# Optimization experiments

Measured on AMD Instinct MI355X. Metric: run time of the kernel, lower is better.

## Reference

```python
import jax, jax.numpy as jnp
import numpy as np

NUM_CAPSULE = 10
DIM_CAPSULE = 16
ROUTINGS = 3
EPS = 1e-7  # K.epsilon()


def squash(x, axis=-1):
    # bojone squash: x / sqrt(s2 + eps) * s2 / (1 + s2)
    s2 = jnp.sum(jnp.square(x), axis=axis, keepdims=True)
    return x * s2 / ((1.0 + s2) * jnp.sqrt(s2 + EPS))


def setup_inputs() -> dict:
    key = jax.random.key(0)
    k1, k2 = jax.random.split(key)
    B, N, D_in = 64, 2048, 128  # batch, input_num_capsule, input_dim_capsule
    u_vecs = jax.random.normal(k1, (B, N, D_in), dtype=jnp.float32)
    fan_out = NUM_CAPSULE * DIM_CAPSULE
    limit = float(np.sqrt(6.0 / (D_in + fan_out)))  # glorot_uniform
    W = jax.random.uniform(k2, (D_in, fan_out), dtype=jnp.float32,
                           minval=-limit, maxval=limit)
    return {"u_vecs": u_vecs, "W": W}


def reference(u_vecs, W):
    B, N, _ = u_vecs.shape
    # share_weights=True: conv1d with kernel size 1 == matmul over feature dim
    u_hat = (u_vecs @ W).reshape(B, N, NUM_CAPSULE, DIM_CAPSULE)
    u_hat = jnp.transpose(u_hat, (0, 2, 1, 3))  # (B, J, N, D)
    b = jnp.zeros((B, NUM_CAPSULE, N), dtype=u_vecs.dtype)
    o = jnp.zeros((B, NUM_CAPSULE, DIM_CAPSULE), dtype=u_vecs.dtype)
    for i in range(ROUTINGS):
        c = jax.nn.softmax(b, axis=1)           # softmax over output capsules
        o = jnp.einsum('bjn,bjnd->bjd', c, u_hat)
        if i < ROUTINGS - 1:
            b = jnp.einsum('bjd,bjnd->bjn', o, u_hat)  # agreement update
    return squash(o)
```

## Files before the change

### kernel.cpp

```cpp
#include <hip/hip_runtime.h>
#include <math.h>


#define BATCH 64
#define NN    2048
#define KD    128
#define JCAP  10
#define DCAP  16
#define JDIM  160
#define EPSQ  1e-7f
#define TPB   256

#define WS_SP   0
#define WS_GP1  65536
#define WS_O2P  720896
#define WS_V0   802816
#define WS_V1   884736
#define WS_CNT  966656

__global__ __launch_bounds__(TPB) void k_prep(const float* __restrict__ u,
                                              float* __restrict__ Sp,
                                              unsigned int* __restrict__ cnt) {
  const int b = blockIdx.y, tile = blockIdx.x, t = threadIdx.x;
  if (b == 0 && tile == 0 && t < BATCH) cnt[t] = 0u;
  const int k4 = (t & 31) * 4, rg = t >> 5;
  __shared__ float4 red[256];
  const float* p = u + ((size_t)(b * NN) + tile * 256 + rg * 32) * KD + k4;
  float4 a = make_float4(0.f, 0.f, 0.f, 0.f);
#pragma unroll 4
  for (int r = 0; r < 32; ++r) {
    float4 w = *(const float4*)(p + (size_t)r * KD);
    a.x += w.x; a.y += w.y; a.z += w.z; a.w += w.w;
  }
  red[t] = a;
  __syncthreads();
  if (t < 32) {
    float4 s4 = red[t];
#pragma unroll
    for (int rg2 = 1; rg2 < 8; ++rg2) {
      float4 w = red[rg2 * 32 + t];
      s4.x += w.x; s4.y += w.y; s4.z += w.z; s4.w += w.w;
    }
    *(float4*)&Sp[(size_t)(b * 8 + tile) * KD + t * 4] = s4;
  }
}

__global__ __launch_bounds__(TPB) void k_makeV(const float* __restrict__ ws,
                                               const float* __restrict__ W,
                                               float* __restrict__ V,
                                               int pass) {
  const int b = blockIdx.x, t = threadIdx.x;
  __shared__ float gsum[JCAP * KD];
  __shared__ float o_s[JDIM];
  if (pass == 0) {
    const float* SpB = ws + WS_SP + (size_t)b * 8 * KD;
    if (t < KD) {
      float s = 0.f;
#pragma unroll
      for (int tl = 0; tl < 8; ++tl) s += SpB[tl * KD + t];
      gsum[t] = s * 0.1f;
    }
  } else {
    const float* GpB = ws + WS_GP1 + (size_t)b * 8 * (JCAP * KD);
    for (int i = t; i < JCAP * KD; i += TPB) {
      float s = 0.f;
#pragma unroll
      for (int tl = 0; tl < 8; ++tl) s += GpB[(size_t)tl * (JCAP * KD) + i];
      gsum[i] = s;
    }
  }
  __syncthreads();
  if (t < JDIM) {
    const int j = t >> 4;
    const float* gs = pass == 0 ? gsum : (gsum + j * KD);
    float acc = 0.f;
#pragma unroll 4
    for (int k = 0; k < KD; ++k) acc += gs[k] * W[k * JDIM + t];
    o_s[t] = acc;
  }
  __syncthreads();
  const int k = t & 127, gg = t >> 7;
#pragma unroll
  for (int i = 0; i < 5; ++i) {
    const int j = gg * 5 + i;
    const float* wp = W + k * JDIM + j * DCAP;
    float acc = 0.f;
#pragma unroll
    for (int d = 0; d < DCAP; ++d) acc += wp[d] * o_s[j * DCAP + d];
    V[(size_t)(b * JCAP + j) * KD + k] = acc;
  }
}

__global__ __launch_bounds__(TPB) void k_route(const float* __restrict__ u,
                                               const float* __restrict__ V,
                                               const float* __restrict__ W,
                                               float* __restrict__ dst,
                                               float* __restrict__ out,
                                               unsigned int* __restrict__ cnt,
                                               int pass) {
  const int b = blockIdx.y, tile = blockIdx.x, t = threadIdx.x;
  const int r0 = tile * 256;
  __shared__ __align__(16) float Cs[JCAP][260];
  __shared__ __align__(16) float Gp[4][JCAP][KD];
  __shared__ float o_s[JDIM];
  __shared__ float sc[JCAP];
  __shared__ unsigned int lastflag;

  {
    const float* up = u + (size_t)(b * NN + r0 + t) * KD;
    const float* vb = V + (size_t)(b * JCAP) * KD;
    float acc[JCAP];
#pragma unroll
    for (int j = 0; j < JCAP; ++j) acc[j] = 0.f;
    for (int kc = 0; kc < KD; kc += 8) {
      float4 xa = *(const float4*)(up + kc);
      float4 xb = *(const float4*)(up + kc + 4);
#pragma unroll
      for (int j = 0; j < JCAP; ++j) {
        float4 v0 = *(const float4*)(vb + j * KD + kc);
        float4 v1 = *(const float4*)(vb + j * KD + kc + 4);
        acc[j] += xa.x * v0.x + xa.y * v0.y + xa.z * v0.z + xa.w * v0.w
                + xb.x * v1.x + xb.y * v1.y + xb.z * v1.z + xb.w * v1.w;
      }
    }
    float m = acc[0];
#pragma unroll
    for (int j = 1; j < JCAP; ++j) m = fmaxf(m, acc[j]);
    float s = 0.f;
#pragma unroll
    for (int j = 0; j < JCAP; ++j) { acc[j] = __expf(acc[j] - m); s += acc[j]; }
    const float inv = 1.f / s;
#pragma unroll
    for (int j = 0; j < JCAP; ++j) Cs[j][t] = acc[j] * inv;
  }
  __syncthreads();

  {
    const int wave = t >> 6, lane = t & 63;
    const int rw = wave * 64;
    float g0[JCAP], g1[JCAP];
#pragma unroll
    for (int j = 0; j < JCAP; ++j) { g0[j] = 0.f; g1[j] = 0.f; }
    const float* ub = u + (size_t)(b * NN + r0 + rw) * KD + 2 * lane;
    for (int rc = 0; rc < 64; rc += 4) {
      float ua[4], uc[4];
#pragma unroll
      for (int q = 0; q < 4; ++q) {
        float2 w = *(const float2*)(ub + (size_t)(rc + q) * KD);
        ua[q] = w.x; uc[q] = w.y;
      }
#pragma unroll
      for (int j = 0; j < JCAP; ++j) {
        float4 c4 = *(const float4*)&Cs[j][rw + rc];
        g0[j] += c4.x * ua[0] + c4.y * ua[1] + c4.z * ua[2] + c4.w * ua[3];
        g1[j] += c4.x * uc[0] + c4.y * uc[1] + c4.z * uc[2] + c4.w * uc[3];
      }
    }
#pragma unroll
    for (int j = 0; j < JCAP; ++j)
      *(float2*)&Gp[wave][j][2 * lane] = make_float2(g0[j], g1[j]);
  }
  __syncthreads();

  if (pass == 0) {
    float* g1d = dst + (size_t)(b * 8 + tile) * (JCAP * KD);
    for (int i = t; i < JCAP * KD; i += TPB)
      g1d[i] = Gp[0][0][i] + Gp[1][0][i] + Gp[2][0][i] + Gp[3][0][i];
    return;
  }

  for (int i = t; i < JCAP * KD; i += TPB)
    Gp[0][0][i] = Gp[0][0][i] + Gp[1][0][i] + Gp[2][0][i] + Gp[3][0][i];
  __syncthreads();
  if (t < JDIM) {
    const int j = t >> 4;
    float acc = 0.f;
#pragma unroll 4
    for (int k = 0; k < KD; ++k) acc += Gp[0][j][k] * W[k * JDIM + t];
    dst[(size_t)(b * 8 + tile) * JDIM + t] = acc;
  }
  __syncthreads();
  if (t == 0) {
    __threadfence();
    lastflag = atomicAdd(&cnt[b], 1u);
  }
  __syncthreads();
  if (lastflag != 7u) return;
  __threadfence();

  const float* p = dst + (size_t)b * 8 * JDIM;
  if (t < JDIM) {
    float s = 0.f;
#pragma unroll
    for (int tl = 0; tl < 8; ++tl) s += p[tl * JDIM + t];
    o_s[t] = s;
  }
  __syncthreads();
  if (t < JCAP) {
    float s2 = 0.f;
#pragma unroll
    for (int d = 0; d < DCAP; ++d) { float x = o_s[t * DCAP + d]; s2 += x * x; }
    sc[t] = s2 / ((1.f + s2) * sqrtf(s2 + EPSQ));
  }
  __syncthreads();
  if (t < JDIM) out[b * JDIM + t] = o_s[t] * sc[t >> 4];
}

extern "C" void kernel_launch(void* const* d_in, const int* in_sizes, int n_in,
                              void* d_out, int out_size, void* d_ws, size_t ws_size,
                              hipStream_t stream) {
  const float* u = (const float*)d_in[0];
  const float* W = (const float*)d_in[1];
  float* out = (float*)d_out;
  float* ws  = (float*)d_ws;

  float* Sp  = ws + WS_SP;
  float* Gp1 = ws + WS_GP1;
  float* O2p = ws + WS_O2P;
  float* V0  = ws + WS_V0;
  float* V1  = ws + WS_V1;
  unsigned int* cnt = (unsigned int*)(ws + WS_CNT);

  k_prep <<<dim3(8, BATCH), TPB, 0, stream>>>(u, Sp, cnt);
  k_makeV<<<BATCH, TPB, 0, stream>>>(ws, W, V0, 0);
  k_route<<<dim3(8, BATCH), TPB, 0, stream>>>(u, V0, W, Gp1, out, cnt, 0);
  k_makeV<<<BATCH, TPB, 0, stream>>>(ws, W, V1, 1);
  k_route<<<dim3(8, BATCH), TPB, 0, stream>>>(u, V1, W, O2p, out, cnt, 1);
}
```

Baseline: 195.2 us.

## Transpose u into k-major layout so routing logit loads coalesce

The prep kernel now also writes a transposed copy of u (k-major, n contiguous) to workspace, using a shared-memory tile, while still computing the column sums. The first phase of the routing kernel reads this transposed copy, so lanes load consecutive n for each k instead of each thread reading its own 512-byte row. This removes the strided per-thread row access in the logit computation. The cost is an extra full read and write of u (32 MB each) plus a larger workspace; the second phase still reads the original layout.

```diff
diff --git a/kernel.cpp b/kernel.cpp
--- a/kernel.cpp
+++ b/kernel.cpp
@@ -12,36 +12,50 @@
 #define TPB   256
 
 #define WS_SP   0
-#define WS_GP1  65536
-#define WS_O2P  720896
-#define WS_V0   802816
-#define WS_V1   884736
-#define WS_CNT  966656
-
-__global__ __launch_bounds__(TPB) void k_prep(const float* __restrict__ u,
-                                              float* __restrict__ Sp,
-                                              unsigned int* __restrict__ cnt) {
+#define WS_GP1  262144
+#define WS_O2P  917504
+#define WS_V0   999424
+#define WS_V1   1081344
+#define WS_CNT  1163264
+#define WS_UT   1163328
+
+__global__ __launch_bounds__(TPB) void k_tpose(const float* __restrict__ u,
+                                               float* __restrict__ uT,
+                                               float* __restrict__ Sp,
+                                               unsigned int* __restrict__ cnt) {
   const int b = blockIdx.y, tile = blockIdx.x, t = threadIdx.x;
   if (b == 0 && tile == 0 && t < BATCH) cnt[t] = 0u;
-  const int k4 = (t & 31) * 4, rg = t >> 5;
+  __shared__ __align__(16) float Ts[64][132];
   __shared__ float4 red[256];
-  const float* p = u + ((size_t)(b * NN) + tile * 256 + rg * 32) * KD + k4;
-  float4 a = make_float4(0.f, 0.f, 0.f, 0.f);
-#pragma unroll 4
-  for (int r = 0; r < 32; ++r) {
-    float4 w = *(const float4*)(p + (size_t)r * KD);
-    a.x += w.x; a.y += w.y; a.z += w.z; a.w += w.w;
-  }
-  red[t] = a;
+  const float* src = u + ((size_t)b * NN + tile * 64) * KD;
+  float4 csum = make_float4(0.f, 0.f, 0.f, 0.f);
+#pragma unroll
+  for (int q = 0; q < 8; ++q) {
+    const int idx = t + 256 * q;
+    const int row = idx >> 5, k4 = idx & 31;
+    float4 w = *(const float4*)(src + (size_t)row * KD + k4 * 4);
+    csum.x += w.x; csum.y += w.y; csum.z += w.z; csum.w += w.w;
+    *(float4*)&Ts[row][k4 * 4] = w;
+  }
+  red[t] = csum;
   __syncthreads();
   if (t < 32) {
     float4 s4 = red[t];
 #pragma unroll
-    for (int rg2 = 1; rg2 < 8; ++rg2) {
-      float4 w = red[rg2 * 32 + t];
+    for (int g = 1; g < 8; ++g) {
+      float4 w = red[t + 32 * g];
       s4.x += w.x; s4.y += w.y; s4.z += w.z; s4.w += w.w;
     }
-    *(float4*)&Sp[(size_t)(b * 8 + tile) * KD + t * 4] = s4;
+    *(float4*)&Sp[(size_t)(b * 32 + tile) * KD + t * 4] = s4;
+  }
+  float* dstb = uT + (size_t)b * (NN * KD) + tile * 64;
+#pragma unroll
+  for (int q = 0; q < 8; ++q) {
+    const int idx = t + 256 * q;
+    const int k = idx >> 4, n4 = idx & 15;
+    float4 v = make_float4(Ts[n4 * 4 + 0][k], Ts[n4 * 4 + 1][k],
+                           Ts[n4 * 4 + 2][k], Ts[n4 * 4 + 3][k]);
+    *(float4*)(dstb + (size_t)k * NN + n4 * 4) = v;
   }
 }
 
@@ -53,11 +67,11 @@
   __shared__ float gsum[JCAP * KD];
   __shared__ float o_s[JDIM];
   if (pass == 0) {
-    const float* SpB = ws + WS_SP + (size_t)b * 8 * KD;
+    const float* SpB = ws + WS_SP + (size_t)b * 32 * KD;
     if (t < KD) {
       float s = 0.f;
 #pragma unroll
-      for (int tl = 0; tl < 8; ++tl) s += SpB[tl * KD + t];
+      for (int tl = 0; tl < 32; ++tl) s += SpB[tl * KD + t];
       gsum[t] = s * 0.1f;
     }
   } else {
@@ -92,6 +106,7 @@
 }
 
 __global__ __launch_bounds__(TPB) void k_route(const float* __restrict__ u,
+                                               const float* __restrict__ uT,
                                                const float* __restrict__ V,
                                                const float* __restrict__ W,
                                                float* __restrict__ dst,
@@ -107,20 +122,25 @@
   __shared__ unsigned int lastflag;
 
   {
-    const float* up = u + (size_t)(b * NN + r0 + t) * KD;
+    const float* uTb = uT + (size_t)b * (NN * KD) + r0 + t;
     const float* vb = V + (size_t)(b * JCAP) * KD;
     float acc[JCAP];
 #pragma unroll
     for (int j = 0; j < JCAP; ++j) acc[j] = 0.f;
-    for (int kc = 0; kc < KD; kc += 8) {
-      float4 xa = *(const float4*)(up + kc);
-      float4 xb = *(const float4*)(up + kc + 4);
+    for (int k = 0; k < KD; k += 8) {
+      float x0 = uTb[(size_t)(k + 0) * NN];
+      float x1 = uTb[(size_t)(k + 1) * NN];
+      float x2 = uTb[(size_t)(k + 2) * NN];
+      float x3 = uTb[(size_t)(k + 3) * NN];
+      float x4 = uTb[(size_t)(k + 4) * NN];
+      float x5 = uTb[(size_t)(k + 5) * NN];
+      float x6 = uTb[(size_t)(k + 6) * NN];
+      float x7 = uTb[(size_t)(k + 7) * NN];
 #pragma unroll
       for (int j = 0; j < JCAP; ++j) {
-        float4 v0 = *(const float4*)(vb + j * KD + kc);
-        float4 v1 = *(const float4*)(vb + j * KD + kc + 4);
-        acc[j] += xa.x * v0.x + xa.y * v0.y + xa.z * v0.z + xa.w * v0.w
-                + xb.x * v1.x + xb.y * v1.y + xb.z * v1.z + xb.w * v1.w;
+        const float* vj = vb + j * KD + k;
+        acc[j] += x0 * vj[0] + x1 * vj[1] + x2 * vj[2] + x3 * vj[3]
+                + x4 * vj[4] + x5 * vj[5] + x6 * vj[6] + x7 * vj[7];
       }
     }
     float m = acc[0];
@@ -219,11 +239,12 @@
   float* O2p = ws + WS_O2P;
   float* V0  = ws + WS_V0;
   float* V1  = ws + WS_V1;
+  float* uT  = ws + WS_UT;
   unsigned int* cnt = (unsigned int*)(ws + WS_CNT);
 
-  k_prep <<<dim3(8, BATCH), TPB, 0, stream>>>(u, Sp, cnt);
+  k_tpose<<<dim3(32, BATCH), TPB, 0, stream>>>(u, uT, Sp, cnt);
   k_makeV<<<BATCH, TPB, 0, stream>>>(ws, W, V0, 0);
-  k_route<<<dim3(8, BATCH), TPB, 0, stream>>>(u, V0, W, Gp1, out, cnt, 0);
+  k_route<<<dim3(8, BATCH), TPB, 0, stream>>>(u, uT, V0, W, Gp1, out, cnt, 0);
   k_makeV<<<BATCH, TPB, 0, stream>>>(ws, W, V1, 1);
-  k_route<<<dim3(8, BATCH), TPB, 0, stream>>>(u, V1, W, O2p, out, cnt, 1);
-}
+  k_route<<<dim3(8, BATCH), TPB, 0, stream>>>(u, uT, V1, W, O2p, out, cnt, 1);
+}
```

After: 211.5 us. 1.08x slower.
